# Optimization experiments

Measured on AMD Instinct MI355X. Metric: run time of the kernel, lower is better.

## Reference

```python
import math
import jax, jax.numpy as jnp
import numpy as np

D = 128


def setup_inputs() -> dict:
    key = jax.random.key(0)
    ks = jax.random.split(key, 12)
    B, C, H, W = 8, D, 128, 128
    init_logit = math.log(0.05 / (0.25 - 0.05))
    s = 0.05
    return {
        "u": jax.random.normal(ks[0], (B, C, H, W), jnp.float32),
        "diff_logits": jnp.full((3, C), init_logit, jnp.float32),
        "W1": jax.random.normal(ks[1], (C, 2 * C), jnp.float32) * s,
        "b1": jnp.zeros((2 * C,), jnp.float32),
        "W2": jax.random.normal(ks[2], (2 * C, C), jnp.float32) * s,
        "b2": jnp.zeros((C,), jnp.float32),
        "Wf": jax.random.normal(ks[3], (C, C), jnp.float32) * s,
        "bf": jnp.zeros((C,), jnp.float32),
        "Wi": jax.random.normal(ks[4], (C, C), jnp.float32) * s,
        "bi": jnp.zeros((C,), jnp.float32),
        "Wc": jax.random.normal(ks[5], (C, C), jnp.float32) * s,
        "bc": jnp.zeros((C,), jnp.float32),
        "scale": jnp.ones((C,), jnp.float32),
        "log_dt": jnp.asarray(math.log(0.1), jnp.float32),
        "alpha_mem": jnp.asarray(0.1, jnp.float32),
    }


def _laplacian(u, diff_logits):
    # multi-dilation 5-point stencil with learnable per-channel diffusion
    out = jnp.zeros_like(u)
    for i, d in enumerate((1, 2, 4)):
        coeff = 0.25 * jax.nn.sigmoid(diff_logits[i])  # (C,)
        p = jnp.pad(u, ((0, 0), (0, 0), (d, d), (d, d)), mode="reflect")
        lap = (p[:, :, d:-d, 2 * d:] + p[:, :, d:-d, :-2 * d]
               + p[:, :, 2 * d:, d:-d] + p[:, :, :-2 * d, d:-d] - 4.0 * u)
        out = out + coeff[None, :, None, None] * lap
    return out


def reference(u, diff_logits, W1, b1, W2, b2, Wf, bf, Wi, bi, Wc, bc,
              scale, log_dt, alpha_mem):
    B, C, H, W = u.shape
    dt = jnp.clip(jnp.exp(log_dt), 0.01, 0.3)
    h = jnp.zeros((B, C), u.dtype)
    hist = []
    max_steps = 12
    inv_sqrt_c = 1.0 / np.sqrt(C).astype(np.float32)
    for t in range(max_steps):
        hist.append(jax.lax.stop_gradient(jnp.mean(jnp.abs(u), axis=(0, 2, 3))))
        diff = _laplacian(u, diff_logits)
        # per-cell MLP (channel-last)
        x = u.transpose(0, 2, 3, 1)  # (B,H,W,C)
        react = (jax.nn.gelu(x @ W1 + b1, approximate=False) @ W2 + b2)
        react = react.transpose(0, 3, 1, 2)
        # gated O(1) memory on pooled state
        up = u.mean(axis=(2, 3))  # (B,C)
        h = (h * jax.nn.sigmoid(up @ Wf + bf)
             + jax.nn.sigmoid(up @ Wi + bi) * jnp.tanh(up @ Wc + bc))
        du = diff + react + alpha_mem * h[:, :, None, None]
        u = u + dt * du
        if (t + 1) % 2 == 0:
            x = u.transpose(0, 2, 3, 1)
            rms = jnp.linalg.norm(x, axis=-1, keepdims=True) * inv_sqrt_c
            x = x / (rms + 1e-6) * scale
            u = x.transpose(0, 3, 1, 2)
    channel_history = jnp.stack(hist)  # (T,C)
    channel_velocity = jnp.abs(channel_history[1:] - channel_history[:-1]).mean(axis=0)
    return u, channel_velocity, channel_history, dt
```

## Files before the change

### kernel.cpp

```cpp
#include <hip/hip_runtime.h>


typedef __attribute__((ext_vector_type(8))) short  bf16x8;
typedef __attribute__((ext_vector_type(4))) float  f32x4;

#define VEL_OFF   16777216
#define HIST_OFF  16777344
#define DT_OFF    16778880

#define WS_PSUM   0
#define WS_PABS   262144
#define WS_W1P    524288
#define WS_W2P    540672
#define WS_COEFF  557056
#define WS_H      557440
#define WS_SAB    558464

__device__ __forceinline__ unsigned short f2bf(float x) {
  unsigned int u = __float_as_uint(x);
  u += 0x7FFFu + ((u >> 16) & 1u);
  return (unsigned short)(u >> 16);
}

__device__ __forceinline__ float gelu_fast(float x) {
  float x2 = x * x;
  float p  = __builtin_fmaf(0.044715f, x2, 1.0f);
  float z  = (-1.5957691216057308f * x) * p;
  float t  = __expf(z);
  return x * __builtin_amdgcn_rcpf(1.0f + t);
}

__device__ __forceinline__ int swzB(int px, int c) {
  return px * 128 + (c ^ (((px >> 2) & 3) << 4));
}

__global__ __launch_bounds__(256) void prep_kernel(
    const float* __restrict__ W1, const float* __restrict__ W2,
    const float* __restrict__ dl,
    unsigned short* __restrict__ w1p, unsigned short* __restrict__ w2p,
    float* __restrict__ coeff)
{
  int id = blockIdx.x * 256 + threadIdx.x;
  if (id < 4096) {
    int lane = id & 63, t2 = id >> 6;
    int kt = t2 & 3, nt = t2 >> 2;
    int n  = nt * 16 + (lane & 15);
    int k0 = kt * 32 + (lane >> 4) * 8;
#pragma unroll
    for (int e = 0; e < 8; e++) w1p[id * 8 + e] = f2bf(W1[(k0 + e) * 256 + n]);
  } else if (id < 8192) {
    int id2 = id - 4096;
    int lane = id2 & 63, t2 = id2 >> 6;
    int ks = t2 & 7, nt = t2 >> 3;
    int n  = nt * 16 + (lane & 15);
    int k0 = ks * 32 + (lane >> 4) * 8;
#pragma unroll
    for (int e = 0; e < 8; e++) w2p[id2 * 8 + e] = f2bf(W2[(k0 + e) * 128 + n]);
  } else if (id < 8192 + 384) {
    int j = id - 8192;
    coeff[j] = 0.25f / (1.f + expf(-dl[j]));
  }
}

__global__ __launch_bounds__(256) void transpose_kernel(
    const float* __restrict__ uin, float* __restrict__ uout,
    float* __restrict__ psum, float* __restrict__ pabs)
{
  int bh = blockIdx.x;
  int b = bh >> 7, h = bh & 127;
  int t = threadIdx.x;
  int c = t & 127, wh = t >> 7;
  const float* inb = uin + (size_t)((b * 128 + c) * 128 + h) * 128;
  float* outb = uout + (size_t)((b * 128 + h) * 128) * 128 + c;
  float s = 0.f, sa = 0.f;
#pragma unroll 4
  for (int i = 0; i < 16; i++) {
    int w4 = wh * 16 + i;
    f32x4 v = *(const f32x4*)(inb + w4 * 4);
#pragma unroll
    for (int k = 0; k < 4; k++) {
      float x = v[k];
      s += x; sa += fabsf(x);
      outb[(w4 * 4 + k) * 128] = x;
    }
  }
  int rem = h * 2 + wh;
  psum[(size_t)(b * 256 + rem) * 128 + c] = s;
  pabs[(size_t)(b * 256 + rem) * 128 + c] = sa;
}

__global__ __launch_bounds__(512) void gate_kernel(
    const float* __restrict__ psum, const float* __restrict__ pabs,
    const float* __restrict__ Wf, const float* __restrict__ bfv,
    const float* __restrict__ Wi, const float* __restrict__ biv,
    const float* __restrict__ Wc, const float* __restrict__ bcv,
    float* __restrict__ hbuf, float* __restrict__ sab, int step_t)
{
  __shared__ float red_s[4][128];
  __shared__ float red_a[4][128];
  __shared__ float up_l[128];
  __shared__ float gl[3][128];

  int b = blockIdx.x;
  int tid = threadIdx.x;
  int c = tid & 127, q = tid >> 7;

  const float* ps = psum + (size_t)b * 256 * 128;
  const float* pa = pabs + (size_t)b * 256 * 128;
  float s = 0.f, sa = 0.f;
#pragma unroll 8
  for (int j = 0; j < 64; j++) {
    int r = q * 64 + j;
    s  += ps[r * 128 + c];
    sa += pa[r * 128 + c];
  }
  red_s[q][c] = s; red_a[q][c] = sa;
  __syncthreads();
  if (q == 0) {
    s  = red_s[0][c] + red_s[1][c] + red_s[2][c] + red_s[3][c];
    sa = red_a[0][c] + red_a[1][c] + red_a[2][c] + red_a[3][c];
    up_l[c] = s * (1.f / 16384.f);
    sab[(step_t * 8 + b) * 128 + c] = sa;
  }
  __syncthreads();
  if (q < 3) {
    const float* W = (q == 0) ? Wf : ((q == 1) ? Wi : Wc);
    float acc = 0.f;
#pragma unroll 8
    for (int k = 0; k < 128; k++) acc += up_l[k] * W[k * 128 + c];
    gl[q][c] = acc;
  }
  __syncthreads();
  if (q == 0) {
    float hp = (step_t == 0) ? 0.f : hbuf[b * 128 + c];
    float fg = 1.f / (1.f + expf(-(gl[0][c] + bfv[c])));
    float ig = 1.f / (1.f + expf(-(gl[1][c] + biv[c])));
    float cg = tanhf(gl[2][c] + bcv[c]);
    hbuf[b * 128 + c] = hp * fg + ig * cg;
  }
}

template<bool RMS, bool OUT_BCHW, bool ACCUM>
__global__ __launch_bounds__(256, 2) void step_kernel(
    const float* __restrict__ src, float* __restrict__ dst,
    const unsigned short* __restrict__ w1p, const unsigned short* __restrict__ w2p,
    const float* __restrict__ b1g, const float* __restrict__ b2g,
    const float* __restrict__ coeff, const float* __restrict__ hbuf,
    const float* __restrict__ scaleg,
    float* __restrict__ psum, float* __restrict__ pabs,
    const float* __restrict__ log_dt_p, const float* __restrict__ alpha_p)
{
  __shared__ __align__(16) unsigned short ldsA[64 * 256];
  __shared__ __align__(16) float ldsB[64 * 128];
  float* rmsbuf = ((float*)ldsA) + 6144;

  const int tid  = threadIdx.x;
  const int lane = tid & 63;
  const int wv   = tid >> 6;
  const int lm   = lane & 15;
  const int lk   = lane >> 4;

  int bid = blockIdx.x;
  int wg  = (bid & 7) * 256 + (bid >> 3);
  int b   = wg >> 8;
  int rem = wg & 255;
  int h   = rem >> 1;
  int w0  = (rem & 1) * 64;

  float dtv = expf(log_dt_p[0]);
  dtv = fminf(fmaxf(dtv, 0.01f), 0.3f);
  const float am = alpha_p[0];

  const float* __restrict__ srow = src + (size_t)((b * 128 + h) * 128) * 128;

#pragma unroll
  for (int i = 0; i < 8; i++) {
    int j  = i * 256 + tid;
    int px = j >> 5, cq = j & 31;
    int w  = w0 + px;
    const float* pc = srow + w * 128 + cq * 4;
    f32x4 ctr = *(const f32x4*)pc;
    unsigned long long pk =
        (unsigned long long)f2bf(ctr.x)
      | ((unsigned long long)f2bf(ctr.y) << 16)
      | ((unsigned long long)f2bf(ctr.z) << 32)
      | ((unsigned long long)f2bf(ctr.w) << 48);
    *(unsigned long long*)((char*)ldsA + (px * 256 + ((cq * 8) ^ ((px & 7) << 4)))) = pk;
    f32x4 acc = {0.f, 0.f, 0.f, 0.f};
#pragma unroll
    for (int di = 0; di < 3; di++) {
      int d  = 1 << di;
      int wl = w - d; wl = wl < 0 ? -wl : wl;
      int wr = w + d; wr = wr >= 128 ? 254 - wr : wr;
      int hu = h - d; hu = hu < 0 ? -hu : hu;
      int hd = h + d; hd = hd >= 128 ? 254 - hd : hd;
      f32x4 sum = *(const f32x4*)(srow + wl * 128 + cq * 4);
      sum += *(const f32x4*)(srow + wr * 128 + cq * 4);
      sum += *(const f32x4*)(src + (size_t)((b * 128 + hu) * 128 + w) * 128 + cq * 4);
      sum += *(const f32x4*)(src + (size_t)((b * 128 + hd) * 128 + w) * 128 + cq * 4);
      f32x4 cf = *(const f32x4*)(coeff + di * 128 + cq * 4);
      acc += cf * (sum - 4.f * ctr);
    }
    f32x4 pre = ctr + dtv * acc;
    *(f32x4*)(ldsB + swzB(px, cq * 4)) = pre;
  }
  __syncthreads();

  f32x4 acc1[4][4] = {};
#pragma unroll
  for (int ks = 0; ks < 4; ks++) {
    bf16x8 aF[4], bF[4];
#pragma unroll
    for (int mt = 0; mt < 4; mt++) {
      int px = mt * 16 + lm;
      int kb = ks * 64 + lk * 16;
      aF[mt] = *(bf16x8*)((char*)ldsA + (px * 256 + (kb ^ ((px & 7) << 4))));
    }
#pragma unroll
    for (int nt = 0; nt < 4; nt++) {
      int ntg = wv * 4 + nt;
      bF[nt] = *(const bf16x8*)(w1p + (size_t)((ntg * 4 + ks) * 64 + lane) * 8);
    }
#pragma unroll
    for (int mt = 0; mt < 4; mt++)
#pragma unroll
      for (int nt = 0; nt < 4; nt++)
        acc1[mt][nt] = __builtin_amdgcn_mfma_f32_16x16x32_bf16(aF[mt], bF[nt], acc1[mt][nt], 0, 0, 0);
  }
  __syncthreads();

#pragma unroll
  for (int nt = 0; nt < 4; nt++) {
    int n = wv * 64 + nt * 16 + lm;
    float bias = b1g[n];
#pragma unroll
    for (int mt = 0; mt < 4; mt++) {
#pragma unroll
      for (int r = 0; r < 4; r++) {
        float x = acc1[mt][nt][r] + bias;
        float g = gelu_fast(x);
        int px = mt * 16 + lk * 4 + r;
        *(unsigned short*)((char*)ldsA + (px * 512 + ((n * 2) ^ ((px & 7) << 4)))) = f2bf(g);
      }
    }
  }
  __syncthreads();

  f32x4 acc2[4][2] = {};
#pragma unroll
  for (int ks = 0; ks < 8; ks++) {
    bf16x8 aF[4], bF2[2];
#pragma unroll
    for (int mt = 0; mt < 4; mt++) {
      int px = mt * 16 + lm;
      int kb = ks * 64 + lk * 16;
      aF[mt] = *(bf16x8*)((char*)ldsA + (px * 512 + (kb ^ ((px & 7) << 4))));
    }
#pragma unroll
    for (int nt = 0; nt < 2; nt++) {
      int ntg = wv * 2 + nt;
      bF2[nt] = *(const bf16x8*)(w2p + (size_t)((ntg * 8 + ks) * 64 + lane) * 8);
    }
#pragma unroll
    for (int mt = 0; mt < 4; mt++)
#pragma unroll
      for (int nt = 0; nt < 2; nt++)
        acc2[mt][nt] = __builtin_amdgcn_mfma_f32_16x16x32_bf16(aF[mt], bF2[nt], acc2[mt][nt], 0, 0, 0);
  }

#pragma unroll
  for (int nt = 0; nt < 2; nt++) {
    int c = wv * 32 + nt * 16 + lm;
    float b2v = b2g[c];
    float hv  = am * hbuf[b * 128 + c];
#pragma unroll
    for (int mt = 0; mt < 4; mt++) {
#pragma unroll
      for (int r = 0; r < 4; r++) {
        int px  = mt * 16 + lk * 4 + r;
        int idx = swzB(px, c);
        ldsB[idx] = ldsB[idx] + dtv * (acc2[mt][nt][r] + b2v + hv);
      }
    }
  }
  __syncthreads();

  if (RMS) {
    int px = tid >> 2, part = tid & 3;
    float ss = 0.f;
#pragma unroll
    for (int i2 = 0; i2 < 8; i2++) {
      int cb = part * 32 + i2 * 4;
      f32x4 v = *(f32x4*)(ldsB + swzB(px, cb));
      ss += v.x * v.x + v.y * v.y + v.z * v.z + v.w * v.w;
    }
    ss += __shfl_xor(ss, 1);
    ss += __shfl_xor(ss, 2);
    if (part == 0) {
      float rms = sqrtf(ss) * 0.08838834764831845f;
      rmsbuf[px] = 1.f / (rms + 1e-6f);
    }
    __syncthreads();
  }

  if (!OUT_BCHW) {
    float* drow = dst + (size_t)((b * 128 + h) * 128) * 128;
    int cq = tid & 31, p8 = tid >> 5;
    f32x4 scl = {1.f, 1.f, 1.f, 1.f};
    if (RMS) scl = *(const f32x4*)(scaleg + cq * 4);
    f32x4 s4v = {0.f, 0.f, 0.f, 0.f}, a4v = {0.f, 0.f, 0.f, 0.f};
#pragma unroll
    for (int ii = 0; ii < 8; ii++) {
      int px = ii * 8 + p8;
      f32x4 v = *(f32x4*)(ldsB + swzB(px, cq * 4));
      if (RMS) { float iv = rmsbuf[px]; v = v * iv * scl; }
      *(f32x4*)(drow + (size_t)(w0 + px) * 128 + cq * 4) = v;
      if (ACCUM) {
        s4v += v;
        f32x4 av; av.x = fabsf(v.x); av.y = fabsf(v.y); av.z = fabsf(v.z); av.w = fabsf(v.w);
        a4v += av;
      }
    }
    if (ACCUM) {
      float* scratch = (float*)ldsA;
      *(f32x4*)(scratch + (p8 * 32 + cq) * 4) = s4v;
      *(f32x4*)(scratch + 1024 + (p8 * 32 + cq) * 4) = a4v;
      __syncthreads();
      if (tid < 128) {
        int c = tid, cq2 = c >> 2, e = c & 3;
        float s = 0.f, sa = 0.f;
#pragma unroll
        for (int p = 0; p < 8; p++) {
          s  += scratch[(p * 32 + cq2) * 4 + e];
          sa += scratch[1024 + (p * 32 + cq2) * 4 + e];
        }
        psum[(size_t)(b * 256 + rem) * 128 + c] = s;
        pabs[(size_t)(b * 256 + rem) * 128 + c] = sa;
      }
    }
  } else {
#pragma unroll
    for (int ii = 0; ii < 8; ii++) {
      int j = ii * 256 + tid;
      int c = j >> 4, pq = j & 15;
      float sc = scaleg[c];
      f32x4 v;
      v.x = ldsB[swzB(pq * 4 + 0, c)] * rmsbuf[pq * 4 + 0];
      v.y = ldsB[swzB(pq * 4 + 1, c)] * rmsbuf[pq * 4 + 1];
      v.z = ldsB[swzB(pq * 4 + 2, c)] * rmsbuf[pq * 4 + 2];
      v.w = ldsB[swzB(pq * 4 + 3, c)] * rmsbuf[pq * 4 + 3];
      v = v * sc;
      *(f32x4*)(dst + (size_t)(((b * 128 + c) * 128 + h) * 128) + w0 + pq * 4) = v;
    }
  }
}

__global__ __launch_bounds__(128) void vel_kernel(
    const float* __restrict__ sab, const float* __restrict__ log_dt_p,
    float* __restrict__ out)
{
  int c = threadIdx.x;
  float hst[12];
#pragma unroll
  for (int t = 0; t < 12; t++) {
    float x = 0.f;
#pragma unroll
    for (int b = 0; b < 8; b++) x += sab[(t * 8 + b) * 128 + c];
    hst[t] = x * (1.f / 131072.f);
    out[HIST_OFF + t * 128 + c] = hst[t];
  }
  float v = 0.f;
#pragma unroll
  for (int t = 0; t < 11; t++) v += fabsf(hst[t + 1] - hst[t]);
  out[VEL_OFF + c] = v * (1.f / 11.f);
  if (c == 0) {
    float dtv = expf(log_dt_p[0]);
    out[DT_OFF] = fminf(fmaxf(dtv, 0.01f), 0.3f);
  }
}

extern "C" void kernel_launch(void* const* d_in, const int* in_sizes, int n_in,
                              void* d_out, int out_size, void* d_ws, size_t ws_size,
                              hipStream_t stream)
{
  (void)in_sizes; (void)n_in; (void)out_size; (void)ws_size;
  float*       uB     = (float*)d_in[0];
  const float* dlog   = (const float*)d_in[1];
  const float* W1     = (const float*)d_in[2];
  const float* b1     = (const float*)d_in[3];
  const float* W2     = (const float*)d_in[4];
  const float* b2     = (const float*)d_in[5];
  const float* Wf     = (const float*)d_in[6];
  const float* bf_    = (const float*)d_in[7];
  const float* Wi     = (const float*)d_in[8];
  const float* bi     = (const float*)d_in[9];
  const float* Wc     = (const float*)d_in[10];
  const float* bc     = (const float*)d_in[11];
  const float* scale  = (const float*)d_in[12];
  const float* log_dt = (const float*)d_in[13];
  const float* alpha  = (const float*)d_in[14];

  float* out = (float*)d_out;
  float* ws  = (float*)d_ws;

  float* psum  = ws + WS_PSUM;
  float* pabs  = ws + WS_PABS;
  unsigned short* w1p = (unsigned short*)(ws + WS_W1P);
  unsigned short* w2p = (unsigned short*)(ws + WS_W2P);
  float* coeff = ws + WS_COEFF;
  float* hbuf  = ws + WS_H;
  float* sab   = ws + WS_SAB;

  prep_kernel<<<34, 256, 0, stream>>>(W1, W2, dlog, w1p, w2p, coeff);
  transpose_kernel<<<1024, 256, 0, stream>>>(uB, out, psum, pabs);

  for (int t = 0; t < 12; t++) {
    gate_kernel<<<8, 512, 0, stream>>>(psum, pabs, Wf, bf_, Wi, bi, Wc, bc,
                                       hbuf, sab, t);
    const float* s = (t & 1) ? uB  : out;
    float*       d = (t & 1) ? out : uB;
    if (t == 11) {
      step_kernel<true, true, false><<<2048, 256, 0, stream>>>(
          s, d, w1p, w2p, b1, b2, coeff, hbuf, scale, psum, pabs, log_dt, alpha);
    } else if (t & 1) {
      step_kernel<true, false, true><<<2048, 256, 0, stream>>>(
          s, d, w1p, w2p, b1, b2, coeff, hbuf, scale, psum, pabs, log_dt, alpha);
    } else {
      step_kernel<false, false, true><<<2048, 256, 0, stream>>>(
          s, d, w1p, w2p, b1, b2, coeff, hbuf, scale, psum, pabs, log_dt, alpha);
    }
  }
  vel_kernel<<<1, 128, 0, stream>>>(sab, log_dt, out);
}
```

Measured before the change: 1.046 ms.

## Double step-kernel block to 512 threads, halving per-wave MFMA tiles

The fused step kernel now runs 512 threads per block instead of 256, so each of 8 waves owns half as many output columns in both GEMMs. This cuts accumulator registers per wave and raises waves per CU. The stencil, RMS and output loops are remapped to the wider block, and the stencil coefficients are hoisted out of the pixel loop. Each A fragment read from LDS is now reused across fewer MFMAs, so LDS traffic per FLOP goes up, and there are more waves contending at each barrier.

```diff
diff --git a/kernel.cpp b/kernel.cpp
--- a/kernel.cpp
+++ b/kernel.cpp
@@ -141,7 +141,7 @@
 }
 
 template<bool RMS, bool OUT_BCHW, bool ACCUM>
-__global__ __launch_bounds__(256, 2) void step_kernel(
+__global__ __launch_bounds__(512, 4) void step_kernel(
     const float* __restrict__ src, float* __restrict__ dst,
     const unsigned short* __restrict__ w1p, const unsigned short* __restrict__ w2p,
     const float* __restrict__ b1g, const float* __restrict__ b2g,
@@ -173,43 +173,49 @@
 
   const float* __restrict__ srow = src + (size_t)((b * 128 + h) * 128) * 128;
 
-#pragma unroll
-  for (int i = 0; i < 8; i++) {
-    int j  = i * 256 + tid;
-    int px = j >> 5, cq = j & 31;
-    int w  = w0 + px;
-    const float* pc = srow + w * 128 + cq * 4;
-    f32x4 ctr = *(const f32x4*)pc;
-    unsigned long long pk =
-        (unsigned long long)f2bf(ctr.x)
-      | ((unsigned long long)f2bf(ctr.y) << 16)
-      | ((unsigned long long)f2bf(ctr.z) << 32)
-      | ((unsigned long long)f2bf(ctr.w) << 48);
-    *(unsigned long long*)((char*)ldsA + (px * 256 + ((cq * 8) ^ ((px & 7) << 4)))) = pk;
-    f32x4 acc = {0.f, 0.f, 0.f, 0.f};
-#pragma unroll
-    for (int di = 0; di < 3; di++) {
-      int d  = 1 << di;
-      int wl = w - d; wl = wl < 0 ? -wl : wl;
-      int wr = w + d; wr = wr >= 128 ? 254 - wr : wr;
-      int hu = h - d; hu = hu < 0 ? -hu : hu;
-      int hd = h + d; hd = hd >= 128 ? 254 - hd : hd;
-      f32x4 sum = *(const f32x4*)(srow + wl * 128 + cq * 4);
-      sum += *(const f32x4*)(srow + wr * 128 + cq * 4);
-      sum += *(const f32x4*)(src + (size_t)((b * 128 + hu) * 128 + w) * 128 + cq * 4);
-      sum += *(const f32x4*)(src + (size_t)((b * 128 + hd) * 128 + w) * 128 + cq * 4);
-      f32x4 cf = *(const f32x4*)(coeff + di * 128 + cq * 4);
-      acc += cf * (sum - 4.f * ctr);
-    }
-    f32x4 pre = ctr + dtv * acc;
-    *(f32x4*)(ldsB + swzB(px, cq * 4)) = pre;
-  }
-  __syncthreads();
-
-  f32x4 acc1[4][4] = {};
+  {
+    const int cq = tid & 31;
+    const int pxb = tid >> 5;
+    f32x4 cf0 = *(const f32x4*)(coeff + 0 * 128 + cq * 4);
+    f32x4 cf1 = *(const f32x4*)(coeff + 1 * 128 + cq * 4);
+    f32x4 cf2 = *(const f32x4*)(coeff + 2 * 128 + cq * 4);
+#pragma unroll
+    for (int i = 0; i < 4; i++) {
+      int px = i * 16 + pxb;
+      int w  = w0 + px;
+      const float* pc = srow + w * 128 + cq * 4;
+      f32x4 ctr = *(const f32x4*)pc;
+      unsigned long long pk =
+          (unsigned long long)f2bf(ctr.x)
+        | ((unsigned long long)f2bf(ctr.y) << 16)
+        | ((unsigned long long)f2bf(ctr.z) << 32)
+        | ((unsigned long long)f2bf(ctr.w) << 48);
+      *(unsigned long long*)((char*)ldsA + (px * 256 + ((cq * 8) ^ ((px & 7) << 4)))) = pk;
+      f32x4 acc = {0.f, 0.f, 0.f, 0.f};
+#pragma unroll
+      for (int di = 0; di < 3; di++) {
+        int d  = 1 << di;
+        int wl = w - d; wl = wl < 0 ? -wl : wl;
+        int wr = w + d; wr = wr >= 128 ? 254 - wr : wr;
+        int hu = h - d; hu = hu < 0 ? -hu : hu;
+        int hd = h + d; hd = hd >= 128 ? 254 - hd : hd;
+        f32x4 sum = *(const f32x4*)(srow + wl * 128 + cq * 4);
+        sum += *(const f32x4*)(srow + wr * 128 + cq * 4);
+        sum += *(const f32x4*)(src + (size_t)((b * 128 + hu) * 128 + w) * 128 + cq * 4);
+        sum += *(const f32x4*)(src + (size_t)((b * 128 + hd) * 128 + w) * 128 + cq * 4);
+        f32x4 cf = (di == 0) ? cf0 : ((di == 1) ? cf1 : cf2);
+        acc += cf * (sum - 4.f * ctr);
+      }
+      f32x4 pre = ctr + dtv * acc;
+      *(f32x4*)(ldsB + swzB(px, cq * 4)) = pre;
+    }
+  }
+  __syncthreads();
+
+  f32x4 acc1[4][2] = {};
 #pragma unroll
   for (int ks = 0; ks < 4; ks++) {
-    bf16x8 aF[4], bF[4];
+    bf16x8 aF[4], bF[2];
 #pragma unroll
     for (int mt = 0; mt < 4; mt++) {
       int px = mt * 16 + lm;
@@ -217,21 +223,21 @@
       aF[mt] = *(bf16x8*)((char*)ldsA + (px * 256 + (kb ^ ((px & 7) << 4))));
     }
 #pragma unroll
-    for (int nt = 0; nt < 4; nt++) {
-      int ntg = wv * 4 + nt;
+    for (int nt = 0; nt < 2; nt++) {
+      int ntg = wv * 2 + nt;
       bF[nt] = *(const bf16x8*)(w1p + (size_t)((ntg * 4 + ks) * 64 + lane) * 8);
     }
 #pragma unroll
     for (int mt = 0; mt < 4; mt++)
 #pragma unroll
-      for (int nt = 0; nt < 4; nt++)
+      for (int nt = 0; nt < 2; nt++)
         acc1[mt][nt] = __builtin_amdgcn_mfma_f32_16x16x32_bf16(aF[mt], bF[nt], acc1[mt][nt], 0, 0, 0);
   }
   __syncthreads();
 
 #pragma unroll
-  for (int nt = 0; nt < 4; nt++) {
-    int n = wv * 64 + nt * 16 + lm;
+  for (int nt = 0; nt < 2; nt++) {
+    int n = wv * 32 + nt * 16 + lm;
     float bias = b1g[n];
 #pragma unroll
     for (int mt = 0; mt < 4; mt++) {
@@ -246,31 +252,24 @@
   }
   __syncthreads();
 
-  f32x4 acc2[4][2] = {};
+  f32x4 acc2[4] = {};
 #pragma unroll
   for (int ks = 0; ks < 8; ks++) {
-    bf16x8 aF[4], bF2[2];
+    bf16x8 aF[4], bF2;
 #pragma unroll
     for (int mt = 0; mt < 4; mt++) {
       int px = mt * 16 + lm;
       int kb = ks * 64 + lk * 16;
       aF[mt] = *(bf16x8*)((char*)ldsA + (px * 512 + (kb ^ ((px & 7) << 4))));
     }
-#pragma unroll
-    for (int nt = 0; nt < 2; nt++) {
-      int ntg = wv * 2 + nt;
-      bF2[nt] = *(const bf16x8*)(w2p + (size_t)((ntg * 8 + ks) * 64 + lane) * 8);
-    }
+    bF2 = *(const bf16x8*)(w2p + (size_t)((wv * 8 + ks) * 64 + lane) * 8);
 #pragma unroll
     for (int mt = 0; mt < 4; mt++)
-#pragma unroll
-      for (int nt = 0; nt < 2; nt++)
-        acc2[mt][nt] = __builtin_amdgcn_mfma_f32_16x16x32_bf16(aF[mt], bF2[nt], acc2[mt][nt], 0, 0, 0);
-  }
-
-#pragma unroll
-  for (int nt = 0; nt < 2; nt++) {
-    int c = wv * 32 + nt * 16 + lm;
+      acc2[mt] = __builtin_amdgcn_mfma_f32_16x16x32_bf16(aF[mt], bF2, acc2[mt], 0, 0, 0);
+  }
+
+  {
+    int c = wv * 16 + lm;
     float b2v = b2g[c];
     float hv  = am * hbuf[b * 128 + c];
 #pragma unroll
@@ -279,23 +278,24 @@
       for (int r = 0; r < 4; r++) {
         int px  = mt * 16 + lk * 4 + r;
         int idx = swzB(px, c);
-        ldsB[idx] = ldsB[idx] + dtv * (acc2[mt][nt][r] + b2v + hv);
+        ldsB[idx] = ldsB[idx] + dtv * (acc2[mt][r] + b2v + hv);
       }
     }
   }
   __syncthreads();
 
   if (RMS) {
-    int px = tid >> 2, part = tid & 3;
+    int px = tid >> 3, part = tid & 7;
     float ss = 0.f;
 #pragma unroll
-    for (int i2 = 0; i2 < 8; i2++) {
-      int cb = part * 32 + i2 * 4;
+    for (int i2 = 0; i2 < 4; i2++) {
+      int cb = part * 16 + i2 * 4;
       f32x4 v = *(f32x4*)(ldsB + swzB(px, cb));
       ss += v.x * v.x + v.y * v.y + v.z * v.z + v.w * v.w;
     }
     ss += __shfl_xor(ss, 1);
     ss += __shfl_xor(ss, 2);
+    ss += __shfl_xor(ss, 4);
     if (part == 0) {
       float rms = sqrtf(ss) * 0.08838834764831845f;
       rmsbuf[px] = 1.f / (rms + 1e-6f);
@@ -305,13 +305,13 @@
 
   if (!OUT_BCHW) {
     float* drow = dst + (size_t)((b * 128 + h) * 128) * 128;
-    int cq = tid & 31, p8 = tid >> 5;
+    int cq = tid & 31, p16 = tid >> 5;
     f32x4 scl = {1.f, 1.f, 1.f, 1.f};
     if (RMS) scl = *(const f32x4*)(scaleg + cq * 4);
     f32x4 s4v = {0.f, 0.f, 0.f, 0.f}, a4v = {0.f, 0.f, 0.f, 0.f};
 #pragma unroll
-    for (int ii = 0; ii < 8; ii++) {
-      int px = ii * 8 + p8;
+    for (int ii = 0; ii < 4; ii++) {
+      int px = ii * 16 + p16;
       f32x4 v = *(f32x4*)(ldsB + swzB(px, cq * 4));
       if (RMS) { float iv = rmsbuf[px]; v = v * iv * scl; }
       *(f32x4*)(drow + (size_t)(w0 + px) * 128 + cq * 4) = v;
@@ -323,16 +323,16 @@
     }
     if (ACCUM) {
       float* scratch = (float*)ldsA;
-      *(f32x4*)(scratch + (p8 * 32 + cq) * 4) = s4v;
-      *(f32x4*)(scratch + 1024 + (p8 * 32 + cq) * 4) = a4v;
+      *(f32x4*)(scratch + (p16 * 32 + cq) * 4) = s4v;
+      *(f32x4*)(scratch + 2048 + (p16 * 32 + cq) * 4) = a4v;
       __syncthreads();
       if (tid < 128) {
         int c = tid, cq2 = c >> 2, e = c & 3;
         float s = 0.f, sa = 0.f;
 #pragma unroll
-        for (int p = 0; p < 8; p++) {
+        for (int p = 0; p < 16; p++) {
           s  += scratch[(p * 32 + cq2) * 4 + e];
-          sa += scratch[1024 + (p * 32 + cq2) * 4 + e];
+          sa += scratch[2048 + (p * 32 + cq2) * 4 + e];
         }
         psum[(size_t)(b * 256 + rem) * 128 + c] = s;
         pabs[(size_t)(b * 256 + rem) * 128 + c] = sa;
@@ -340,8 +340,8 @@
     }
   } else {
 #pragma unroll
-    for (int ii = 0; ii < 8; ii++) {
-      int j = ii * 256 + tid;
+    for (int ii = 0; ii < 4; ii++) {
+      int j = ii * 512 + tid;
       int c = j >> 4, pq = j & 15;
       float sc = scaleg[c];
       f32x4 v;
@@ -420,13 +420,13 @@
     const float* s = (t & 1) ? uB  : out;
     float*       d = (t & 1) ? out : uB;
     if (t == 11) {
-      step_kernel<true, true, false><<<2048, 256, 0, stream>>>(
+      step_kernel<true, true, false><<<2048, 512, 0, stream>>>(
           s, d, w1p, w2p, b1, b2, coeff, hbuf, scale, psum, pabs, log_dt, alpha);
     } else if (t & 1) {
-      step_kernel<true, false, true><<<2048, 256, 0, stream>>>(
+      step_kernel<true, false, true><<<2048, 512, 0, stream>>>(
           s, d, w1p, w2p, b1, b2, coeff, hbuf, scale, psum, pabs, log_dt, alpha);
     } else {
-      step_kernel<false, false, true><<<2048, 256, 0, stream>>>(
+      step_kernel<false, false, true><<<2048, 512, 0, stream>>>(
           s, d, w1p, w2p, b1, b2, coeff, hbuf, scale, psum, pabs, log_dt, alpha);
     }
   }
```

Result: faster. 993.8 us (-5.0%).
